# Performance work log

Hardware: AMD Instinct MI355X
Metric: run time of the kernel (lower is better)

The kernel has to match this reference:

```python
import jax, jax.numpy as jnp
import numpy as np

B, T, F = 1024, 512, 64
P, H = 64, 128  # proj_dim, hidden_size


def _init(key, shape, scale):
    return jax.random.normal(key, shape, dtype=jnp.float32) * scale


def setup_inputs() -> dict:
    key = jax.random.key(0)
    ks = jax.random.split(key, 20)
    sp = 1.0 / np.sqrt(P)
    sh = 1.0 / np.sqrt(H)
    return {
        "x": jax.random.normal(ks[0], (B, T, F), dtype=jnp.float32),
        "lengths": jax.random.randint(ks[1], (B,), 1, T, dtype=jnp.int64),
        # input projection
        "W_proj": _init(ks[2], (P, F), 1.0 / np.sqrt(F)),
        "b_proj": jnp.zeros((P,), jnp.float32),
        # LSTM layer 0 (input P -> hidden H), pytorch gate order i,f,g,o
        "W_ih0": _init(ks[3], (4 * H, P), sh),
        "W_hh0": _init(ks[4], (4 * H, H), sh),
        "b_ih0": _init(ks[5], (4 * H,), sh),
        "b_hh0": _init(ks[6], (4 * H,), sh),
        # LSTM layer 1 (input H -> hidden H)
        "W_ih1": _init(ks[7], (4 * H, H), sh),
        "W_hh1": _init(ks[8], (4 * H, H), sh),
        "b_ih1": _init(ks[9], (4 * H,), sh),
        "b_hh1": _init(ks[10], (4 * H,), sh),
        # MLP head: H -> H//2 -> 1 (dropout is identity in eval)
        "W_h1": _init(ks[11], (H // 2, H), sh),
        "b_h1": jnp.zeros((H // 2,), jnp.float32),
        "W_h2": _init(ks[12], (1, H // 2), 1.0 / np.sqrt(H // 2)),
        "b_h2": jnp.zeros((1,), jnp.float32),
    }


def lstm_layer(x_seq, W_ih, W_hh, b_ih, b_hh):
    # x_seq: [B, T, D]; precompute input contribution for all timesteps
    Hh = W_hh.shape[1]
    xg = jnp.einsum("btd,gd->btg", x_seq, W_ih) + b_ih + b_hh  # [B, T, 4H]
    xg_t = jnp.transpose(xg, (1, 0, 2))  # [T, B, 4H]
    Bn = x_seq.shape[0]
    h0 = jnp.zeros((Bn, Hh), x_seq.dtype)
    c0 = jnp.zeros((Bn, Hh), x_seq.dtype)

    def step(carry, g_in):
        h, c = carry
        g = g_in + h @ W_hh.T
        i, f, gg, o = jnp.split(g, 4, axis=-1)
        i = jax.nn.sigmoid(i)
        f = jax.nn.sigmoid(f)
        gg = jnp.tanh(gg)
        o = jax.nn.sigmoid(o)
        c = f * c + i * gg
        h = o * jnp.tanh(c)
        return (h, c), h

    _, hs = jax.lax.scan(step, (h0, c0), xg_t)  # hs: [T, B, H]
    return jnp.transpose(hs, (1, 0, 2))  # [B, T, H]


def reference(x, lengths, W_proj, b_proj, W_ih0, W_hh0, b_ih0, b_hh0,
              W_ih1, W_hh1, b_ih1, b_hh1, W_h1, b_h1, W_h2, b_h2):
    # eval mode: dropout layers are identity
    proj = jnp.einsum("btf,pf->btp", x, W_proj) + b_proj  # [B, T, P]
    h1 = lstm_layer(proj, W_ih0, W_hh0, b_ih0, b_hh0)
    h2 = lstm_layer(h1, W_ih1, W_hh1, b_ih1, b_hh1)
    last = h2[:, -1, :]  # [B, H]
    hid = jax.nn.relu(last @ W_h1.T + b_h1)
    logits = (hid @ W_h2.T + b_h2).squeeze(-1)  # [B]
    return logits
```

## Files before the change

### kernel.cpp

```cpp
#include <hip/hip_runtime.h>
#include <hip/hip_bf16.h>
#include <stdint.h>

typedef __bf16 bf16x8 __attribute__((ext_vector_type(8)));
typedef float  f32x4  __attribute__((ext_vector_type(4)));

#define BAR()  asm volatile("s_waitcnt lgkmcnt(0)\n\ts_barrier" ::: "memory")
#define SB()   __builtin_amdgcn_sched_barrier(0)

static __device__ __forceinline__ float sigm(float x) {
  return __builtin_amdgcn_rcpf(1.0f + __builtin_amdgcn_exp2f(x * -1.4426950408889634f));
}
static __device__ __forceinline__ float tanh_fast(float x) {
  return 1.0f - 2.0f * __builtin_amdgcn_rcpf(1.0f + __builtin_amdgcn_exp2f(x * 2.8853900817779268f));
}
static __device__ __forceinline__ unsigned short f2bf(float f) {
  return __builtin_bit_cast(unsigned short, (__bf16)f);
}
static __device__ __forceinline__ float bf2f(unsigned short u) {
  union { uint32_t i; float f; } v; v.i = ((uint32_t)u) << 16; return v.f;
}
static __device__ __forceinline__ void async16(const float* g, float* l) {
  __builtin_amdgcn_global_load_lds((__attribute__((address_space(1))) void*)g,
                                   (__attribute__((address_space(3))) void*)l, 16, 0, 0);
}

__global__ __launch_bounds__(512) __attribute__((amdgpu_waves_per_eu(2, 2)))
void fraud_lstm_kernel(
    const float* __restrict__ x,     const float* __restrict__ Wproj,
    const float* __restrict__ bproj, const float* __restrict__ Wih0,
    const float* __restrict__ Whh0,  const float* __restrict__ bih0,
    const float* __restrict__ bhh0,  const float* __restrict__ Wih1,
    const float* __restrict__ Whh1,  const float* __restrict__ bih1,
    const float* __restrict__ bhh1,  const float* __restrict__ Wh1,
    const float* __restrict__ bh1,   const float* __restrict__ Wh2,
    const float* __restrict__ bh2,   float* __restrict__ out)
{
  __shared__ unsigned short sWf[65536];
  __shared__ unsigned short sH0f[2][2048];
  __shared__ unsigned short sH1f[2][2048];
  __shared__ float sXB[3*1024];

  const int tid  = threadIdx.x;
  const int lane = tid & 63;
  const int wid  = tid >> 6;
  const int lr   = lane & 15;
  const int lg   = lane >> 4;
  const int b0   = blockIdx.x * 16;
  const int g0   = wid*16 + lr;

  {
    float* sWp = reinterpret_cast<float*>(sWf);
    for (int i = tid; i < 4096; i += 512) sWp[i] = Wproj[i];
  }
  BAR();

  float w0a[2][4][8];
  #pragma unroll
  for (int kk = 0; kk < 2; ++kk)
    #pragma unroll
    for (int n = 0; n < 4; ++n)
      #pragma unroll
      for (int j = 0; j < 8; ++j) w0a[kk][n][j] = 0.f;
  float bacc[4] = {0.f, 0.f, 0.f, 0.f};
  {
    const float* sWp = reinterpret_cast<const float*>(sWf);
    #pragma unroll 2
    for (int p = 0; p < 64; ++p) {
      float av[4];
      #pragma unroll
      for (int n = 0; n < 4; ++n) av[n] = Wih0[(n*128 + g0)*64 + p];
      float bp = bproj[p];
      #pragma unroll
      for (int n = 0; n < 4; ++n) bacc[n] += av[n] * bp;
      #pragma unroll
      for (int kk = 0; kk < 2; ++kk) {
        f32x4 wa = *(const f32x4*)&sWp[p*64 + kk*32 + lg*8];
        f32x4 wb = *(const f32x4*)&sWp[p*64 + kk*32 + lg*8 + 4];
        #pragma unroll
        for (int n = 0; n < 4; ++n)
          #pragma unroll
          for (int j = 0; j < 4; ++j) {
            w0a[kk][n][j]     += av[n] * wa[j];
            w0a[kk][n][4 + j] += av[n] * wb[j];
          }
      }
    }
  }
  bf16x8 w0f[2][4];
  #pragma unroll
  for (int kk = 0; kk < 2; ++kk)
    #pragma unroll
    for (int n = 0; n < 4; ++n)
      #pragma unroll
      for (int j = 0; j < 8; ++j) w0f[kk][n][j] = (__bf16)w0a[kk][n][j];

  float b0r[4], b1r[4];
  #pragma unroll
  for (int n = 0; n < 4; ++n) {
    const int g = n*128 + g0;
    b0r[n] = bih0[g] + bhh0[g] + bacc[n];
    b1r[n] = bih1[g] + bhh1[g];
  }
  BAR();

  bf16x8 whh0[4][4], wih1[4][4];
  #pragma unroll
  for (int n = 0; n < 4; ++n)
    #pragma unroll
    for (int kk = 0; kk < 4; ++kk) {
      const int ro = (n*128 + g0)*128 + kk*32 + lg*8;
      const float* p0 = Whh0 + ro;
      const float* p1 = Wih1 + ro;
      #pragma unroll
      for (int j = 0; j < 8; ++j) {
        whh0[n][kk][j] = (__bf16)p0[j];
        wih1[n][kk][j] = (__bf16)p1[j];
      }
    }
  #pragma unroll
  for (int n = 0; n < 4; ++n)
    #pragma unroll
    for (int kk = 0; kk < 4; ++kk) {
      const int ro = (n*128 + g0)*128 + kk*32 + lg*8;
      const float* p2 = Whh1 + ro;
      bf16x8 w;
      #pragma unroll
      for (int j = 0; j < 8; ++j) w[j] = (__bf16)p2[j];
      *(bf16x8*)&sWf[((wid*16 + n*4 + kk)*64 + lane)*8] = w;
    }

  for (int i = tid; i < 2048; i += 512) {
    sH0f[0][i] = 0; sH0f[1][i] = 0; sH1f[0][i] = 0; sH1f[1][i] = 0;
  }

  const float* xw = x + (size_t)(b0 + (lane & 15)) * (512*64)
                      + ((wid >> 1) & 1) * 32 + (lane >> 4) * 8 + (wid & 1) * 4;
  if (wid < 4) {
    async16(xw,      &sXB[0*1024 + wid*256]);
    async16(xw + 64, &sXB[1*1024 + wid*256]);
    asm volatile("s_waitcnt vmcnt(1)" ::: "memory");
  }
  BAR();

  const int hwb = (g0 >> 5)*1024 + ((g0 >> 3) & 3)*256 + (g0 & 7)*2 + lg*64;
  const int lb  = lane * 16;

  f32x4 c0r = {0.f,0.f,0.f,0.f}, c1r = {0.f,0.f,0.f,0.f};
  int bufR = 0, bufW = 2;

  #pragma unroll 1
  for (int t = 0; t < 512; ++t) {
    const int cur = t & 1;

    if (wid < 4 && t < 510) async16(xw + (t + 2)*64, &sXB[bufW*1024 + wid*256]);

    f32x4 acc0[4];
    #pragma unroll
    for (int n = 0; n < 4; ++n) acc0[n] = f32x4{b0r[n], b0r[n], b0r[n], b0r[n]};
    const char* xp = (const char*)sXB + bufR*4096 + lb;
    #pragma unroll
    for (int kk = 0; kk < 2; ++kk) {
      f32x4 a0 = *(const f32x4*)(xp + kk*2048);
      f32x4 a1 = *(const f32x4*)(xp + kk*2048 + 1024);
      bf16x8 xa;
      #pragma unroll
      for (int j = 0; j < 4; ++j) { xa[j] = (__bf16)a0[j]; xa[4+j] = (__bf16)a1[j]; }
      #pragma unroll
      for (int n = 0; n < 4; ++n)
        acc0[n] = __builtin_amdgcn_mfma_f32_16x16x32_bf16(xa, w0f[kk][n], acc0[n], 0, 0, 0);
      SB();
    }
    const char* h0p = (const char*)sH0f[cur ^ 1] + lb;
    #pragma unroll
    for (int kk = 0; kk < 4; ++kk) {
      bf16x8 ha = *(const bf16x8*)(h0p + kk*1024);
      #pragma unroll
      for (int n = 0; n < 4; ++n)
        acc0[n] = __builtin_amdgcn_mfma_f32_16x16x32_bf16(ha, whh0[n][kk], acc0[n], 0, 0, 0);
      SB();
    }
    {
      char* hw = (char*)sH0f[cur] + hwb;
      #pragma unroll
      for (int r = 0; r < 4; ++r) {
        float iv = sigm(acc0[0][r]);
        float fv = sigm(acc0[1][r]);
        float gv = tanh_fast(acc0[2][r]);
        float ov = sigm(acc0[3][r]);
        float c  = fv * c0r[r] + iv * gv;
        c0r[r] = c;
        *(unsigned short*)(hw + r*16) = f2bf(ov * tanh_fast(c));
      }
    }
    SB();
    f32x4 acc1[4];
    #pragma unroll
    for (int n = 0; n < 4; ++n) acc1[n] = f32x4{b1r[n], b1r[n], b1r[n], b1r[n]};
    #pragma unroll
    for (int kk = 0; kk < 4; ++kk) {
      bf16x8 ha = *(const bf16x8*)(h0p + kk*1024);
      #pragma unroll
      for (int n = 0; n < 4; ++n)
        acc1[n] = __builtin_amdgcn_mfma_f32_16x16x32_bf16(ha, wih1[n][kk], acc1[n], 0, 0, 0);
      SB();
    }
    const char* h1p = (const char*)sH1f[cur] + lb;
    const char* wp  = (const char*)sWf + wid*16384 + lb;
    #pragma unroll
    for (int kk = 0; kk < 4; ++kk) {
      bf16x8 ha = *(const bf16x8*)(h1p + kk*1024);
      #pragma unroll
      for (int n = 0; n < 4; ++n) {
        bf16x8 wf = *(const bf16x8*)(wp + (n*4 + kk)*1024);
        acc1[n] = __builtin_amdgcn_mfma_f32_16x16x32_bf16(ha, wf, acc1[n], 0, 0, 0);
      }
      SB();
    }
    if (t > 0) {
      char* hw = (char*)sH1f[cur ^ 1] + hwb;
      #pragma unroll
      for (int r = 0; r < 4; ++r) {
        float iv = sigm(acc1[0][r]);
        float fv = sigm(acc1[1][r]);
        float gv = tanh_fast(acc1[2][r]);
        float ov = sigm(acc1[3][r]);
        float c  = fv * c1r[r] + iv * gv;
        c1r[r] = c;
        *(unsigned short*)(hw + r*16) = f2bf(ov * tanh_fast(c));
      }
    }

    if (wid < 4) {
      if (t < 510) asm volatile("s_waitcnt vmcnt(1)" ::: "memory");
      else         asm volatile("s_waitcnt vmcnt(0)" ::: "memory");
    }
    BAR();

    bufR = (bufR == 2) ? 0 : bufR + 1;
    bufW = (bufW == 2) ? 0 : bufW + 1;
  }

  {
    f32x4 acc1[4];
    #pragma unroll
    for (int n = 0; n < 4; ++n) acc1[n] = f32x4{b1r[n], b1r[n], b1r[n], b1r[n]};
    const char* h0p = (const char*)sH0f[1] + lb;
    #pragma unroll
    for (int kk = 0; kk < 4; ++kk) {
      bf16x8 ha = *(const bf16x8*)(h0p + kk*1024);
      #pragma unroll
      for (int n = 0; n < 4; ++n)
        acc1[n] = __builtin_amdgcn_mfma_f32_16x16x32_bf16(ha, wih1[n][kk], acc1[n], 0, 0, 0);
    }
    const char* h1p = (const char*)sH1f[0] + lb;
    const char* wp  = (const char*)sWf + wid*16384 + lb;
    #pragma unroll
    for (int kk = 0; kk < 4; ++kk) {
      bf16x8 ha = *(const bf16x8*)(h1p + kk*1024);
      #pragma unroll
      for (int n = 0; n < 4; ++n) {
        bf16x8 wf = *(const bf16x8*)(wp + (n*4 + kk)*1024);
        acc1[n] = __builtin_amdgcn_mfma_f32_16x16x32_bf16(ha, wf, acc1[n], 0, 0, 0);
      }
    }
    char* hw = (char*)sH1f[1] + hwb;
    #pragma unroll
    for (int r = 0; r < 4; ++r) {
      float iv = sigm(acc1[0][r]);
      float fv = sigm(acc1[1][r]);
      float gv = tanh_fast(acc1[2][r]);
      float ov = sigm(acc1[3][r]);
      float c  = fv * c1r[r] + iv * gv;
      c1r[r] = c;
      *(unsigned short*)(hw + r*16) = f2bf(ov * tanh_fast(c));
    }
    BAR();
  }

  {
    int row = tid >> 5;
    int j0  = (tid & 31) * 2;
    float a0 = bh1[j0], a1 = bh1[j0 + 1];
    const float* w0 = Wh1 + j0*128;
    const float* w1 = w0 + 128;
    #pragma unroll 8
    for (int k = 0; k < 128; ++k) {
      float hv = bf2f(sH1f[1][(k >> 5)*512 + ((k >> 3) & 3)*128 + row*8 + (k & 7)]);
      a0 += hv * w0[k];
      a1 += hv * w1[k];
    }
    sXB[row*64 + j0]     = fmaxf(a0, 0.f);
    sXB[row*64 + j0 + 1] = fmaxf(a1, 0.f);
  }
  BAR();
  if (tid < 16) {
    float a = bh2[0];
    #pragma unroll 8
    for (int j = 0; j < 64; ++j) a += sXB[tid*64 + j] * Wh2[j];
    out[b0 + tid] = a;
  }
}

extern "C" void kernel_launch(void* const* d_in, const int* in_sizes, int n_in,
                              void* d_out, int out_size, void* d_ws, size_t ws_size,
                              hipStream_t stream) {
  (void)in_sizes; (void)n_in; (void)d_ws; (void)ws_size; (void)out_size;
  const float* x     = (const float*)d_in[0];
  const float* Wproj = (const float*)d_in[2];
  const float* bproj = (const float*)d_in[3];
  const float* Wih0  = (const float*)d_in[4];
  const float* Whh0  = (const float*)d_in[5];
  const float* bih0  = (const float*)d_in[6];
  const float* bhh0  = (const float*)d_in[7];
  const float* Wih1  = (const float*)d_in[8];
  const float* Whh1  = (const float*)d_in[9];
  const float* bih1  = (const float*)d_in[10];
  const float* bhh1  = (const float*)d_in[11];
  const float* Wh1   = (const float*)d_in[12];
  const float* bh1   = (const float*)d_in[13];
  const float* Wh2   = (const float*)d_in[14];
  const float* bh2   = (const float*)d_in[15];
  float* out = (float*)d_out;

  hipLaunchKernelGGL(fraud_lstm_kernel, dim3(64), dim3(512), 0, stream,
                     x, Wproj, bproj, Wih0, Whh0, bih0, bhh0,
                     Wih1, Whh1, bih1, bhh1, Wh1, bh1, Wh2, bh2, out);
}
```

Before: 1.126 ms.

## Interleave layer-0 gate activations with layer-1 MFMAs and hoist LDS loads

Restructures the per-timestep body so that all LDS operand loads (x, h0, h1, W_hh1 fragments) are issued up front or double-buffered ahead of use. The layer-0 pointwise gate math and h0 store are split per row and interleaved between the layer-1 recurrent MFMA groups. This hides transcendental VALU latency behind matrix-core work and LDS latency behind MFMAs, at the cost of more live registers under a fixed two-waves-per-EU budget.

```diff
diff --git a/kernel.cpp b/kernel.cpp
--- a/kernel.cpp
+++ b/kernel.cpp
@@ -24,6 +24,11 @@
   __builtin_amdgcn_global_load_lds((__attribute__((address_space(1))) void*)g,
                                    (__attribute__((address_space(3))) void*)l, 16, 0, 0);
 }
+
+#define PW0(r) { float iv=sigm(acc0[0][r]); float fv=sigm(acc0[1][r]); \
+  float gv=tanh_fast(acc0[2][r]); float ov=sigm(acc0[3][r]); \
+  float c=fv*c0r[r]+iv*gv; c0r[r]=c; \
+  *(unsigned short*)(hw0+(r)*16)=f2bf(ov*tanh_fast(c)); }
 
 __global__ __launch_bounds__(512) __attribute__((amdgpu_waves_per_eu(2, 2)))
 void fraud_lstm_kernel(
@@ -155,68 +160,117 @@
 
     if (wid < 4 && t < 510) async16(xw + (t + 2)*64, &sXB[bufW*1024 + wid*256]);
 
-    f32x4 acc0[4];
-    #pragma unroll
-    for (int n = 0; n < 4; ++n) acc0[n] = f32x4{b0r[n], b0r[n], b0r[n], b0r[n]};
-    const char* xp = (const char*)sXB + bufR*4096 + lb;
-    #pragma unroll
-    for (int kk = 0; kk < 2; ++kk) {
-      f32x4 a0 = *(const f32x4*)(xp + kk*2048);
-      f32x4 a1 = *(const f32x4*)(xp + kk*2048 + 1024);
-      bf16x8 xa;
-      #pragma unroll
-      for (int j = 0; j < 4; ++j) { xa[j] = (__bf16)a0[j]; xa[4+j] = (__bf16)a1[j]; }
-      #pragma unroll
-      for (int n = 0; n < 4; ++n)
-        acc0[n] = __builtin_amdgcn_mfma_f32_16x16x32_bf16(xa, w0f[kk][n], acc0[n], 0, 0, 0);
-      SB();
-    }
+    const char* xp  = (const char*)sXB + bufR*4096 + lb;
     const char* h0p = (const char*)sH0f[cur ^ 1] + lb;
-    #pragma unroll
-    for (int kk = 0; kk < 4; ++kk) {
-      bf16x8 ha = *(const bf16x8*)(h0p + kk*1024);
-      #pragma unroll
-      for (int n = 0; n < 4; ++n)
-        acc0[n] = __builtin_amdgcn_mfma_f32_16x16x32_bf16(ha, whh0[n][kk], acc0[n], 0, 0, 0);
-      SB();
-    }
-    {
-      char* hw = (char*)sH0f[cur] + hwb;
-      #pragma unroll
-      for (int r = 0; r < 4; ++r) {
-        float iv = sigm(acc0[0][r]);
-        float fv = sigm(acc0[1][r]);
-        float gv = tanh_fast(acc0[2][r]);
-        float ov = sigm(acc0[3][r]);
-        float c  = fv * c0r[r] + iv * gv;
-        c0r[r] = c;
-        *(unsigned short*)(hw + r*16) = f2bf(ov * tanh_fast(c));
-      }
-    }
-    SB();
-    f32x4 acc1[4];
-    #pragma unroll
-    for (int n = 0; n < 4; ++n) acc1[n] = f32x4{b1r[n], b1r[n], b1r[n], b1r[n]};
-    #pragma unroll
-    for (int kk = 0; kk < 4; ++kk) {
-      bf16x8 ha = *(const bf16x8*)(h0p + kk*1024);
-      #pragma unroll
-      for (int n = 0; n < 4; ++n)
-        acc1[n] = __builtin_amdgcn_mfma_f32_16x16x32_bf16(ha, wih1[n][kk], acc1[n], 0, 0, 0);
-      SB();
-    }
     const char* h1p = (const char*)sH1f[cur] + lb;
     const char* wp  = (const char*)sWf + wid*16384 + lb;
-    #pragma unroll
-    for (int kk = 0; kk < 4; ++kk) {
-      bf16x8 ha = *(const bf16x8*)(h1p + kk*1024);
-      #pragma unroll
-      for (int n = 0; n < 4; ++n) {
-        bf16x8 wf = *(const bf16x8*)(wp + (n*4 + kk)*1024);
-        acc1[n] = __builtin_amdgcn_mfma_f32_16x16x32_bf16(ha, wf, acc1[n], 0, 0, 0);
-      }
+    char* hw0 = (char*)sH0f[cur] + hwb;
+
+    f32x4 xv0 = *(const f32x4*)(xp);
+    f32x4 xv1 = *(const f32x4*)(xp + 1024);
+    f32x4 xv2 = *(const f32x4*)(xp + 2048);
+    f32x4 xv3 = *(const f32x4*)(xp + 3072);
+    bf16x8 h0a0 = *(const bf16x8*)(h0p);
+    bf16x8 h0a1 = *(const bf16x8*)(h0p + 1024);
+    bf16x8 h0a2 = *(const bf16x8*)(h0p + 2048);
+    bf16x8 h0a3 = *(const bf16x8*)(h0p + 3072);
+
+    f32x4 acc0[4];
+    #pragma unroll
+    for (int n = 0; n < 4; ++n) acc0[n] = f32x4{b0r[n], b0r[n], b0r[n], b0r[n]};
+    {
+      bf16x8 xa, xb;
+      #pragma unroll
+      for (int j = 0; j < 4; ++j) {
+        xa[j] = (__bf16)xv0[j]; xa[4+j] = (__bf16)xv1[j];
+        xb[j] = (__bf16)xv2[j]; xb[4+j] = (__bf16)xv3[j];
+      }
+      #pragma unroll
+      for (int n = 0; n < 4; ++n)
+        acc0[n] = __builtin_amdgcn_mfma_f32_16x16x32_bf16(xa, w0f[0][n], acc0[n], 0, 0, 0);
+      #pragma unroll
+      for (int n = 0; n < 4; ++n)
+        acc0[n] = __builtin_amdgcn_mfma_f32_16x16x32_bf16(xb, w0f[1][n], acc0[n], 0, 0, 0);
+    }
+    #pragma unroll
+    for (int n = 0; n < 4; ++n)
+      acc0[n] = __builtin_amdgcn_mfma_f32_16x16x32_bf16(h0a0, whh0[n][0], acc0[n], 0, 0, 0);
+    #pragma unroll
+    for (int n = 0; n < 4; ++n)
+      acc0[n] = __builtin_amdgcn_mfma_f32_16x16x32_bf16(h0a1, whh0[n][1], acc0[n], 0, 0, 0);
+    #pragma unroll
+    for (int n = 0; n < 4; ++n)
+      acc0[n] = __builtin_amdgcn_mfma_f32_16x16x32_bf16(h0a2, whh0[n][2], acc0[n], 0, 0, 0);
+    #pragma unroll
+    for (int n = 0; n < 4; ++n)
+      acc0[n] = __builtin_amdgcn_mfma_f32_16x16x32_bf16(h0a3, whh0[n][3], acc0[n], 0, 0, 0);
+    SB();
+
+    bf16x8 h1a0 = *(const bf16x8*)(h1p);
+    bf16x8 h1a1 = *(const bf16x8*)(h1p + 1024);
+    bf16x8 h1a2 = *(const bf16x8*)(h1p + 2048);
+    bf16x8 h1a3 = *(const bf16x8*)(h1p + 3072);
+    bf16x8 wfa0 = *(const bf16x8*)(wp);
+    bf16x8 wfa1 = *(const bf16x8*)(wp + 4096);
+    bf16x8 wfa2 = *(const bf16x8*)(wp + 8192);
+    bf16x8 wfa3 = *(const bf16x8*)(wp + 12288);
+
+    f32x4 acc1[4];
+    #pragma unroll
+    for (int n = 0; n < 4; ++n) acc1[n] = f32x4{b1r[n], b1r[n], b1r[n], b1r[n]};
+    #pragma unroll
+    for (int n = 0; n < 4; ++n)
+      acc1[n] = __builtin_amdgcn_mfma_f32_16x16x32_bf16(h0a0, wih1[n][0], acc1[n], 0, 0, 0);
+    #pragma unroll
+    for (int n = 0; n < 4; ++n)
+      acc1[n] = __builtin_amdgcn_mfma_f32_16x16x32_bf16(h0a1, wih1[n][1], acc1[n], 0, 0, 0);
+    #pragma unroll
+    for (int n = 0; n < 4; ++n)
+      acc1[n] = __builtin_amdgcn_mfma_f32_16x16x32_bf16(h0a2, wih1[n][2], acc1[n], 0, 0, 0);
+    #pragma unroll
+    for (int n = 0; n < 4; ++n)
+      acc1[n] = __builtin_amdgcn_mfma_f32_16x16x32_bf16(h0a3, wih1[n][3], acc1[n], 0, 0, 0);
+    SB();
+
+    {
+      bf16x8 wfb0 = *(const bf16x8*)(wp + 1024);
+      bf16x8 wfb1 = *(const bf16x8*)(wp + 4096 + 1024);
+      bf16x8 wfb2 = *(const bf16x8*)(wp + 8192 + 1024);
+      bf16x8 wfb3 = *(const bf16x8*)(wp + 12288 + 1024);
+      acc1[0] = __builtin_amdgcn_mfma_f32_16x16x32_bf16(h1a0, wfa0, acc1[0], 0, 0, 0);
+      acc1[1] = __builtin_amdgcn_mfma_f32_16x16x32_bf16(h1a0, wfa1, acc1[1], 0, 0, 0);
+      acc1[2] = __builtin_amdgcn_mfma_f32_16x16x32_bf16(h1a0, wfa2, acc1[2], 0, 0, 0);
+      acc1[3] = __builtin_amdgcn_mfma_f32_16x16x32_bf16(h1a0, wfa3, acc1[3], 0, 0, 0);
+      PW0(0);
       SB();
-    }
+      wfa0 = *(const bf16x8*)(wp + 2048);
+      wfa1 = *(const bf16x8*)(wp + 4096 + 2048);
+      wfa2 = *(const bf16x8*)(wp + 8192 + 2048);
+      wfa3 = *(const bf16x8*)(wp + 12288 + 2048);
+      acc1[0] = __builtin_amdgcn_mfma_f32_16x16x32_bf16(h1a1, wfb0, acc1[0], 0, 0, 0);
+      acc1[1] = __builtin_amdgcn_mfma_f32_16x16x32_bf16(h1a1, wfb1, acc1[1], 0, 0, 0);
+      acc1[2] = __builtin_amdgcn_mfma_f32_16x16x32_bf16(h1a1, wfb2, acc1[2], 0, 0, 0);
+      acc1[3] = __builtin_amdgcn_mfma_f32_16x16x32_bf16(h1a1, wfb3, acc1[3], 0, 0, 0);
+      PW0(1);
+      SB();
+      wfb0 = *(const bf16x8*)(wp + 3072);
+      wfb1 = *(const bf16x8*)(wp + 4096 + 3072);
+      wfb2 = *(const bf16x8*)(wp + 8192 + 3072);
+      wfb3 = *(const bf16x8*)(wp + 12288 + 3072);
+      acc1[0] = __builtin_amdgcn_mfma_f32_16x16x32_bf16(h1a2, wfa0, acc1[0], 0, 0, 0);
+      acc1[1] = __builtin_amdgcn_mfma_f32_16x16x32_bf16(h1a2, wfa1, acc1[1], 0, 0, 0);
+      acc1[2] = __builtin_amdgcn_mfma_f32_16x16x32_bf16(h1a2, wfa2, acc1[2], 0, 0, 0);
+      acc1[3] = __builtin_amdgcn_mfma_f32_16x16x32_bf16(h1a2, wfa3, acc1[3], 0, 0, 0);
+      PW0(2);
+      SB();
+      acc1[0] = __builtin_amdgcn_mfma_f32_16x16x32_bf16(h1a3, wfb0, acc1[0], 0, 0, 0);
+      acc1[1] = __builtin_amdgcn_mfma_f32_16x16x32_bf16(h1a3, wfb1, acc1[1], 0, 0, 0);
+      acc1[2] = __builtin_amdgcn_mfma_f32_16x16x32_bf16(h1a3, wfb2, acc1[2], 0, 0, 0);
+      acc1[3] = __builtin_amdgcn_mfma_f32_16x16x32_bf16(h1a3, wfb3, acc1[3], 0, 0, 0);
+      PW0(3);
+      SB();
+    }
+
     if (t > 0) {
       char* hw = (char*)sH1f[cur ^ 1] + hwb;
       #pragma unroll
```

After: 2.050 ms. 82.1% more time.
